# Performance work log

Hardware: AMD Instinct MI355X
Metric: run time of the kernel (lower is better)

## Reference

```python
import jax, jax.numpy as jnp
import numpy as np

N_NODES = 50000
N_EDGES = 800000

def _gcn_layer(x, W, b, src, dst, n):
    # DGL GraphConv, norm='both': out = D_in^{-1/2} A D_out^{-1/2} x W + b
    e = src.shape[0]
    ones = jnp.ones((e,), dtype=x.dtype)
    deg_out = jax.ops.segment_sum(ones, src, num_segments=n)
    deg_in = jax.ops.segment_sum(ones, dst, num_segments=n)
    norm_src = jax.lax.rsqrt(jnp.clip(deg_out, 1.0))  # [n]
    norm_dst = jax.lax.rsqrt(jnp.clip(deg_in, 1.0))   # [n]
    # weight applied before aggregation (in_feats >= out_feats path in DGL)
    h = (x * norm_src[:, None]) @ W                   # [n, out]
    agg = jax.ops.segment_sum(h[src], dst, num_segments=n)  # SpMM: gather-scatter
    return agg * norm_dst[:, None] + b

def setup_inputs() -> dict:
    key = jax.random.key(0)
    ks = jax.random.split(key, 7)
    d_in, d_hid, d_out = 512, 256, 128
    features = jax.random.normal(ks[0], (N_NODES, d_in), dtype=jnp.float32)
    src = jax.random.randint(ks[1], (N_EDGES,), 0, N_NODES, dtype=jnp.int64)
    dst = jax.random.randint(ks[2], (N_EDGES,), 0, N_NODES, dtype=jnp.int64)
    W1 = jax.random.normal(ks[3], (d_in, d_hid), dtype=jnp.float32) / np.sqrt(d_in)
    b1 = jnp.zeros((d_hid,), dtype=jnp.float32)
    W2 = jax.random.normal(ks[4], (d_hid, d_out), dtype=jnp.float32) / np.sqrt(d_hid)
    b2 = jnp.zeros((d_out,), dtype=jnp.float32)
    return {"features": features, "src": src, "dst": dst,
            "W1": W1, "b1": b1, "W2": W2, "b2": b2}

def reference(features, src, dst, W1, b1, W2, b2):
    n = features.shape[0]
    x = _gcn_layer(features, W1, b1, src, dst, n)
    x = jax.nn.relu(x)
    x = _gcn_layer(x, W2, b2, src, dst, n)
    return x
```

## Files before the change

kernel.cpp:

```cpp
#include <hip/hip_runtime.h>
#include <type_traits>

#define DIN  512
#define DHID 256
#define DOF  128

#define RB   13
#define RSZ  (1 << RB)
#define BPR  32

typedef _Float16 f16;
typedef _Float16 f16x8 __attribute__((ext_vector_type(8)));
typedef float f32x4 __attribute__((ext_vector_type(4)));

__global__ __launch_bounds__(256) void hist_deg(const int* __restrict__ src,
                                                const int* __restrict__ dst, int e,
                                                int* __restrict__ cnt_out,
                                                int* __restrict__ cnt_in) {
    __shared__ int h_out[RSZ], h_in[RSZ];
    const int r = blockIdx.x / BPR, b = blockIdx.x % BPR;
    const int base = r << RB;
    const int tid = threadIdx.x;
    for (int j = tid; j < RSZ; j += 256) { h_out[j] = 0; h_in[j] = 0; }
    __syncthreads();

    const int ce = (((e + BPR - 1) / BPR) + 3) & ~3;
    const int s0 = b * ce, s1 = min(s0 + ce, e);
    for (int i = s0 + tid * 4; i < s1; i += 1024) {
        if (i + 3 < s1) {
            int4 sv = *(const int4*)(src + i);
            int4 dv = *(const int4*)(dst + i);
            int v;
            v = sv.x - base; if ((unsigned)v < RSZ) atomicAdd(&h_out[v], 1);
            v = sv.y - base; if ((unsigned)v < RSZ) atomicAdd(&h_out[v], 1);
            v = sv.z - base; if ((unsigned)v < RSZ) atomicAdd(&h_out[v], 1);
            v = sv.w - base; if ((unsigned)v < RSZ) atomicAdd(&h_out[v], 1);
            v = dv.x - base; if ((unsigned)v < RSZ) atomicAdd(&h_in[v], 1);
            v = dv.y - base; if ((unsigned)v < RSZ) atomicAdd(&h_in[v], 1);
            v = dv.z - base; if ((unsigned)v < RSZ) atomicAdd(&h_in[v], 1);
            v = dv.w - base; if ((unsigned)v < RSZ) atomicAdd(&h_in[v], 1);
        } else {
            for (int q = i; q < s1; ++q) {
                int v = src[q] - base; if ((unsigned)v < RSZ) atomicAdd(&h_out[v], 1);
                v = dst[q] - base;     if ((unsigned)v < RSZ) atomicAdd(&h_in[v], 1);
            }
        }
    }
    __syncthreads();
    int* co = cnt_out + (size_t)(r * BPR + b) * RSZ;
    int* ci = cnt_in  + (size_t)(r * BPR + b) * RSZ;
    for (int j = tid; j < RSZ; j += 256) { co[j] = h_out[j]; ci[j] = h_in[j]; }
}

__global__ void sum_base(const int* __restrict__ cnt_out, int* __restrict__ cnt_in,
                         int* __restrict__ deg_in,
                         float* __restrict__ norm_src, float* __restrict__ norm_dst, int n) {
    int d = blockIdx.x * blockDim.x + threadIdx.x;
    if (d >= n) return;
    const int r = d >> RB, j = d & (RSZ - 1);
    int* ci = cnt_in + (size_t)(r * BPR) * RSZ + j;
    int s = 0;
#pragma unroll 4
    for (int b = 0; b < BPR; ++b) {
        int c = ci[(size_t)b * RSZ];
        ci[(size_t)b * RSZ] = s;
        s += c;
    }
    deg_in[d] = s;
    norm_dst[d] = rsqrtf(fmaxf((float)s, 1.0f));
    const int* co = cnt_out + (size_t)(r * BPR) * RSZ + j;
    int s2 = 0;
#pragma unroll 4
    for (int b = 0; b < BPR; ++b) s2 += co[(size_t)b * RSZ];
    norm_src[d] = rsqrtf(fmaxf((float)s2, 1.0f));
}

__global__ __launch_bounds__(256) void scan_part(const int* __restrict__ deg,
                                                 int* __restrict__ partial, int n) {
    const int base = blockIdx.x * 1024;
    const int tid = threadIdx.x;
    int v = 0;
#pragma unroll
    for (int j = 0; j < 4; ++j) {
        int i = base + tid * 4 + j;
        if (i < n) v += deg[i];
    }
    for (int o = 1; o < 64; o <<= 1) v += __shfl_xor(v, o);
    __shared__ int wsum[4];
    if ((tid & 63) == 0) wsum[tid >> 6] = v;
    __syncthreads();
    if (tid == 0) partial[blockIdx.x] = wsum[0] + wsum[1] + wsum[2] + wsum[3];
}

__global__ __launch_bounds__(64) void scan_offsets(int* __restrict__ partial, int nb,
                                                   int* __restrict__ rowptr, int n) {
    const int l = threadIdx.x;
    int orig = (l < nb) ? partial[l] : 0;
    int v = orig;
    for (int o = 1; o < 64; o <<= 1) {
        int u = __shfl_up(v, o);
        if (l >= o) v += u;
    }
    if (l < nb) partial[l] = v - orig;
    if (l == nb - 1) rowptr[n] = v;
}

__global__ __launch_bounds__(256) void scan_apply(const int* __restrict__ deg,
                                                  const int* __restrict__ partial,
                                                  int* __restrict__ rowptr, int n) {
    const int base = blockIdx.x * 1024;
    const int tid = threadIdx.x;
    int x[4]; int s = 0;
#pragma unroll
    for (int j = 0; j < 4; ++j) {
        int i = base + tid * 4 + j;
        x[j] = (i < n) ? deg[i] : 0;
        s += x[j];
    }
    const int l = tid & 63, w = tid >> 6;
    int inc = s;
    for (int o = 1; o < 64; o <<= 1) {
        int u = __shfl_up(inc, o);
        if (l >= o) inc += u;
    }
    __shared__ int wsum[4];
    if (l == 63) wsum[w] = inc;
    __syncthreads();
    int wbase = 0;
    for (int q = 0; q < w; ++q) wbase += wsum[q];
    int excl = partial[blockIdx.x] + wbase + (inc - s);
#pragma unroll
    for (int j = 0; j < 4; ++j) {
        int i = base + tid * 4 + j;
        if (i < n) rowptr[i] = excl;
        excl += x[j];
    }
}

__global__ __launch_bounds__(256) void fill_csr2(const int* __restrict__ src,
                                                 const int* __restrict__ dst, int e,
                                                 const int* __restrict__ rowptr,
                                                 const int* __restrict__ base_in,
                                                 int* __restrict__ csr_src) {
    __shared__ int cur[RSZ];
    const int r = blockIdx.x / BPR, b = blockIdx.x % BPR;
    const int base = r << RB;
    const int tid = threadIdx.x;
    for (int j = tid; j < RSZ; j += 256) cur[j] = 0;
    __syncthreads();

    const int* bi = base_in + (size_t)(r * BPR + b) * RSZ;
    const int ce = (((e + BPR - 1) / BPR) + 3) & ~3;
    const int s0 = b * ce, s1 = min(s0 + ce, e);
    for (int i = s0 + tid * 4; i < s1; i += 1024) {
        if (i + 3 < s1) {
            int4 dv = *(const int4*)(dst + i);
            int4 sv = *(const int4*)(src + i);
            int v;
            v = dv.x - base; if ((unsigned)v < RSZ) { int p = atomicAdd(&cur[v], 1); csr_src[rowptr[base + v] + bi[v] + p] = sv.x; }
            v = dv.y - base; if ((unsigned)v < RSZ) { int p = atomicAdd(&cur[v], 1); csr_src[rowptr[base + v] + bi[v] + p] = sv.y; }
            v = dv.z - base; if ((unsigned)v < RSZ) { int p = atomicAdd(&cur[v], 1); csr_src[rowptr[base + v] + bi[v] + p] = sv.z; }
            v = dv.w - base; if ((unsigned)v < RSZ) { int p = atomicAdd(&cur[v], 1); csr_src[rowptr[base + v] + bi[v] + p] = sv.w; }
        } else {
            for (int q = i; q < s1; ++q) {
                int v = dst[q] - base;
                if ((unsigned)v < RSZ) { int p = atomicAdd(&cur[v], 1); csr_src[rowptr[base + v] + bi[v] + p] = src[q]; }
            }
        }
    }
}

__global__ void transpose_w(const float* __restrict__ W1, const float* __restrict__ W2,
                            f16* __restrict__ w1t, f16* __restrict__ w2t) {
    int t = blockIdx.x * blockDim.x + threadIdx.x;
    if (t < DIN * DHID) {
        int k = t / DHID, c = t % DHID;
        w1t[c * DIN + k] = (f16)W1[t];
    } else {
        int u = t - DIN * DHID;
        if (u < DHID * DOF) {
            int k = u / DOF, c = u % DOF;
            w2t[c * DHID + k] = (f16)W2[u];
        }
    }
}

template<int K, int N, bool A_F32>
__global__ __launch_bounds__(256) void mfma_gemm(const void* __restrict__ Aptr,
                                                 const float* __restrict__ norm,
                                                 const f16* __restrict__ Bt,
                                                 f16* __restrict__ H, int M) {
    constexpr int BM = 128, BN = 128, BK = 32;
    constexpr int NT = K / BK;
    __shared__ __align__(16) f16 smem[BM * BN];

    const int rbase = blockIdx.x * BM;
    const int nbj = blockIdx.y * BN;
    const int tid = threadIdx.x;
    const int l = tid & 63, wid = tid >> 6;
    const int wr = wid >> 1, wc = wid & 1;
    const int fr = l & 15, kg = l >> 4;

    int arow[2], achk[2];
    float ascale[2];
#pragma unroll
    for (int j = 0; j < 2; ++j) {
        int u = tid + j * 256;
        arow[j] = u >> 2; achk[j] = u & 3;
        if (A_F32) {
            int grow = rbase + arow[j];
            ascale[j] = (grow < M) ? norm[grow] : 0.0f;
        }
    }

    struct ABregs {
        float4 a0[2], a1[2];
        f16x8  a16[2];
        f16x8  b[2];
    };

    auto gload = [&](int k0) {
        ABregs r;
#pragma unroll
        for (int j = 0; j < 2; ++j) {
            int grow = rbase + arow[j];
            if (A_F32) {
                if (grow < M) {
                    const float* A = (const float*)Aptr + (long)grow * K + k0 + achk[j] * 8;
                    r.a0[j] = *(const float4*)A;
                    r.a1[j] = *(const float4*)(A + 4);
                } else {
                    r.a0[j] = make_float4(0.f, 0.f, 0.f, 0.f);
                    r.a1[j] = make_float4(0.f, 0.f, 0.f, 0.f);
                }
            } else {
                f16x8 v = {};
                if (grow < M)
                    v = *(const f16x8*)((const f16*)Aptr + (long)grow * K + k0 + achk[j] * 8);
                r.a16[j] = v;
            }
            r.b[j] = *(const f16x8*)(Bt + (long)(nbj + arow[j]) * K + k0 + achk[j] * 8);
        }
        return r;
    };

    auto swrite = [&](int buf, const ABregs& r) {
        f16* As = smem + buf * 8192;
        f16* Bs = As + 4096;
#pragma unroll
        for (int j = 0; j < 2; ++j) {
            f16x8 v;
            if (A_F32) {
                float s = ascale[j];
                v[0] = (f16)(r.a0[j].x * s); v[1] = (f16)(r.a0[j].y * s);
                v[2] = (f16)(r.a0[j].z * s); v[3] = (f16)(r.a0[j].w * s);
                v[4] = (f16)(r.a1[j].x * s); v[5] = (f16)(r.a1[j].y * s);
                v[6] = (f16)(r.a1[j].z * s); v[7] = (f16)(r.a1[j].w * s);
            } else {
                v = r.a16[j];
            }
            int ia = (arow[j] * BK + achk[j] * 8) ^ ((arow[j] & 7) << 3);
            *(f16x8*)&As[ia] = v;
            *(f16x8*)&Bs[ia] = r.b[j];
        }
    };

    f32x4 acc[4][4] = {};

    auto compute = [&](int buf) {
        const f16* As = smem + buf * 8192;
        const f16* Bs = As + 4096;
        f16x8 af[4], bf[4];
#pragma unroll
        for (int m = 0; m < 4; ++m) {
            int row = wr * 64 + m * 16 + fr;
            int ia = (row * BK + kg * 8) ^ ((row & 7) << 3);
            af[m] = *(const f16x8*)&As[ia];
        }
#pragma unroll
        for (int nf = 0; nf < 4; ++nf) {
            int c = wc * 64 + nf * 16 + fr;
            int ib = (c * BK + kg * 8) ^ ((c & 7) << 3);
            bf[nf] = *(const f16x8*)&Bs[ib];
        }
#pragma unroll
        for (int m = 0; m < 4; ++m)
#pragma unroll
            for (int nf = 0; nf < 4; ++nf)
                acc[m][nf] = __builtin_amdgcn_mfma_f32_16x16x32_f16(af[m], bf[nf], acc[m][nf], 0, 0, 0);
    };

    ABregs rb, rc;
    {
        ABregs ra = gload(0);
        swrite(0, ra);
        rb = gload(BK);
        if (NT > 2) rc = gload(2 * BK);
    }

#pragma unroll
    for (int kt = 0; kt < NT; kt += 2) {
        __syncthreads();
        compute(0);
        if (kt + 1 < NT) swrite(1, rb);
        if (kt + 3 < NT) rb = gload((kt + 3) * BK);
        if (kt + 1 < NT) {
            __syncthreads();
            compute(1);
            if (kt + 2 < NT) swrite(0, rc);
            if (kt + 4 < NT) rc = gload((kt + 4) * BK);
        }
    }

    __syncthreads();
#pragma unroll
    for (int m = 0; m < 4; ++m)
#pragma unroll
        for (int nf = 0; nf < 4; ++nf)
#pragma unroll
            for (int i = 0; i < 4; ++i) {
                int row = wr * 64 + m * 16 + (l >> 4) * 4 + i;
                int col = wc * 64 + nf * 16 + (l & 15);
                smem[row * BN + col] = (f16)acc[m][nf][i];
            }
    __syncthreads();
#pragma unroll
    for (int j = 0; j < 8; ++j) {
        int u = tid + j * 256;
        int row = u >> 4, cu = u & 15;
        int grow = rbase + row;
        if (grow < M)
            *(f16x8*)(H + (long)grow * N + nbj + cu * 8) =
                *(const f16x8*)&smem[row * BN + cu * 8];
    }
}

template<int F, bool RELU, bool FOLD, bool OUT_F16>
__global__ __launch_bounds__(256) void aggregate_vec(const f16* __restrict__ H,
                                                     const int* __restrict__ rowptr,
                                                     const int* __restrict__ csr_src,
                                                     const float* __restrict__ norm_dst,
                                                     const float* __restrict__ norm_src,
                                                     const float* __restrict__ bias,
                                                     void* __restrict__ outp, int n) {
    constexpr int LR = F / 8;
    constexpr int EPW = 64 / LR;

    const int node = blockIdx.x * 4 + (threadIdx.x >> 6);
    if (node >= n) return;
    const int l = threadIdx.x & 63;
    const int slot = l / LR;
    const int col = (l & (LR - 1)) * 8;
    const f16* __restrict__ Hc = H + col;

    int k = rowptr[node];
    const int end = rowptr[node + 1];

    float acc[8] = {};
    for (; k + 4 * EPW <= end; k += 4 * EPW) {
        int i0 = csr_src[k + slot];
        int i1 = csr_src[k + EPW + slot];
        int i2 = csr_src[k + 2 * EPW + slot];
        int i3 = csr_src[k + 3 * EPW + slot];
        f16x8 v0 = *(const f16x8*)(Hc + (long)i0 * F);
        f16x8 v1 = *(const f16x8*)(Hc + (long)i1 * F);
        f16x8 v2 = *(const f16x8*)(Hc + (long)i2 * F);
        f16x8 v3 = *(const f16x8*)(Hc + (long)i3 * F);
#pragma unroll
        for (int q = 0; q < 8; ++q) acc[q] += (float)v0[q];
#pragma unroll
        for (int q = 0; q < 8; ++q) acc[q] += (float)v1[q];
#pragma unroll
        for (int q = 0; q < 8; ++q) acc[q] += (float)v2[q];
#pragma unroll
        for (int q = 0; q < 8; ++q) acc[q] += (float)v3[q];
    }
    for (; k < end; k += EPW) {
        int idx = k + slot;
        int ci = min(idx, end - 1);
        int s = csr_src[ci];
        f16x8 v = *(const f16x8*)(Hc + (long)s * F);
        if (idx < end) {
#pragma unroll
            for (int q = 0; q < 8; ++q) acc[q] += (float)v[q];
        }
    }

#pragma unroll
    for (int o = LR; o < 64; o <<= 1) {
#pragma unroll
        for (int q = 0; q < 8; ++q) acc[q] += __shfl_xor(acc[q], o);
    }

    const float nd = norm_dst[node];
    const float ns = FOLD ? norm_src[node] : 1.0f;
#pragma unroll
    for (int q = 0; q < 8; ++q) {
        float v = acc[q] * nd + bias[col + q];
        if (RELU) v = fmaxf(v, 0.0f);
        acc[q] = v * ns;
    }

    if (slot == 0) {
        if (OUT_F16) {
            f16x8 o;
#pragma unroll
            for (int q = 0; q < 8; ++q) o[q] = (f16)acc[q];
            *(f16x8*)((f16*)outp + (long)node * F + col) = o;
        } else {
            float* op = (float*)outp + (long)node * F + col;
            *(float4*)op = make_float4(acc[0], acc[1], acc[2], acc[3]);
            *(float4*)(op + 4) = make_float4(acc[4], acc[5], acc[6], acc[7]);
        }
    }
}

extern "C" void kernel_launch(void* const* d_in, const int* in_sizes, int n_in,
                              void* d_out, int out_size, void* d_ws, size_t ws_size,
                              hipStream_t stream) {
    const float* features = (const float*)d_in[0];
    const int*   src      = (const int*)d_in[1];
    const int*   dst      = (const int*)d_in[2];
    const float* W1       = (const float*)d_in[3];
    const float* b1       = (const float*)d_in[4];
    const float* W2       = (const float*)d_in[5];
    const float* b2       = (const float*)d_in[6];
    float* out = (float*)d_out;

    const int n = in_sizes[0] / DIN;
    const int e = in_sizes[1];

    const int ranges = (n + RSZ - 1) >> RB;
    const size_t cntsz = (size_t)ranges * BPR * RSZ;

    char* ws = (char*)d_ws;
    size_t off = 0;
    auto alloc = [&](size_t bytes) { size_t o = off; off += (bytes + 255) & ~(size_t)255; return o; };
    size_t o_degi   = alloc((size_t)n * 4);
    size_t o_nsrc   = alloc((size_t)n * 4);
    size_t o_ndst   = alloc((size_t)n * 4);
    size_t o_rowptr = alloc((size_t)(n + 1) * 4);
    size_t o_part   = alloc((size_t)64 * 4);
    size_t o_csr    = alloc((size_t)e * 4);
    size_t o_cnto   = alloc(cntsz * 4);
    size_t o_cnti   = alloc(cntsz * 4);
    size_t o_w1t    = alloc((size_t)DIN * DHID * 2);
    size_t o_w2t    = alloc((size_t)DHID * DOF * 2);
    size_t o_h1     = alloc((size_t)n * DHID * 2);
    size_t o_x1     = alloc((size_t)n * DHID * 2);
    size_t o_h2     = alloc((size_t)n * DOF * 2);
    (void)ws_size;

    int*   deg_in   = (int*)(ws + o_degi);
    float* norm_src = (float*)(ws + o_nsrc);
    float* norm_dst = (float*)(ws + o_ndst);
    int*   rowptr   = (int*)(ws + o_rowptr);
    int*   partial  = (int*)(ws + o_part);
    int*   csr_src  = (int*)(ws + o_csr);
    int*   cnt_out  = (int*)(ws + o_cnto);
    int*   cnt_in   = (int*)(ws + o_cnti);
    f16*   w1t      = (f16*)(ws + o_w1t);
    f16*   w2t      = (f16*)(ws + o_w2t);
    f16*   h1       = (f16*)(ws + o_h1);
    f16*   x1       = (f16*)(ws + o_x1);
    f16*   h2       = (f16*)(ws + o_h2);

    const int hblocks = ranges * BPR;
    hist_deg<<<hblocks, 256, 0, stream>>>(src, dst, e, cnt_out, cnt_in);
    sum_base<<<(n + 255) / 256, 256, 0, stream>>>(cnt_out, cnt_in, deg_in,
                                                  norm_src, norm_dst, n);
    const int nb = (n + 1023) / 1024;
    scan_part<<<nb, 256, 0, stream>>>(deg_in, partial, n);
    scan_offsets<<<1, 64, 0, stream>>>(partial, nb, rowptr, n);
    scan_apply<<<nb, 256, 0, stream>>>(deg_in, partial, rowptr, n);
    fill_csr2<<<hblocks, 256, 0, stream>>>(src, dst, e, rowptr, cnt_in, csr_src);
    transpose_w<<<(DIN * DHID + DHID * DOF + 255) / 256, 256, 0, stream>>>(W1, W2, w1t, w2t);

    const int mtiles = (n + 127) / 128;
    const int ablocks = (n + 3) / 4;

    mfma_gemm<DIN, DHID, true><<<dim3(mtiles, DHID / 128), 256, 0, stream>>>(
        features, norm_src, w1t, h1, n);
    aggregate_vec<DHID, true, true, true><<<ablocks, 256, 0, stream>>>(
        h1, rowptr, csr_src, norm_dst, norm_src, b1, x1, n);

    mfma_gemm<DHID, DOF, false><<<dim3(mtiles, DOF / 128), 256, 0, stream>>>(
        x1, nullptr, w2t, h2, n);
    aggregate_vec<DOF, false, false, false><<<ablocks, 256, 0, stream>>>(
        h2, rowptr, csr_src, norm_dst, norm_src, b2, out, n);
}
```

Before: 210.9 us.

## Add LDS-direct double-buffered f16 GEMM for layer 2 and deepen gather unroll

Adds a specialised f16-input GEMM for the second layer that stages A and B tiles straight into LDS with global_load_lds and double buffers them, so loads overlap with MFMA compute. The x1 buffer is padded to a multiple of 128 rows so the kernel can read full tiles without bounds checks. The aggregation loop is also unrolled to 8 outstanding gathers per iteration to expose more memory-level parallelism. The padded rows of x1 are never written, so the GEMM reads uninitialised memory for them; only the output rows beyond n are affected, and those are masked on store. The wider unroll also raises register pressure.

```diff
diff --git a/kernel.cpp b/kernel.cpp
--- a/kernel.cpp
+++ b/kernel.cpp
@@ -12,6 +12,12 @@
 typedef _Float16 f16;
 typedef _Float16 f16x8 __attribute__((ext_vector_type(8)));
 typedef float f32x4 __attribute__((ext_vector_type(4)));
+
+__device__ inline void gload16(const void* g, void* l) {
+    __builtin_amdgcn_global_load_lds(
+        (const __attribute__((address_space(1))) void*)g,
+        (__attribute__((address_space(3))) void*)l, 16, 0, 0);
+}
 
 __global__ __launch_bounds__(256) void hist_deg(const int* __restrict__ src,
                                                 const int* __restrict__ dst, int e,
@@ -335,6 +341,87 @@
     }
 }
 
+template<int K, int N>
+__global__ __launch_bounds__(256) void mfma_gemm16(const f16* __restrict__ A,
+                                                   const f16* __restrict__ Bt,
+                                                   f16* __restrict__ H, int M) {
+    constexpr int BK = 32, NT = K / BK;
+    __shared__ __align__(16) f16 smem[16384];
+    const int rbase = blockIdx.x * 128;
+    const int nbj = blockIdx.y * 128;
+    const int tid = threadIdx.x;
+    const int l = tid & 63, wid = tid >> 6;
+    const int wr = wid >> 1, wc = wid & 1;
+    const int fr = l & 15, kg = l >> 4;
+
+    const int slot0 = wid * 2;
+    const int srow = l >> 2, skch = l & 3;
+
+    auto stage = [&](int buf, int k0) {
+        f16* As = smem + buf * 8192;
+        f16* Bs = As + 4096;
+#pragma unroll
+        for (int q = 0; q < 2; ++q) {
+            int slot = slot0 + q;
+            int row = slot * 16 + srow;
+            const f16* ga = A + (long)(rbase + row) * K + k0 + skch * 8;
+            gload16(ga, As + slot * 512);
+            const f16* gb = Bt + (long)(nbj + row) * K + k0 + skch * 8;
+            gload16(gb, Bs + slot * 512);
+        }
+    };
+
+    f32x4 acc[4][4] = {};
+
+    auto compute = [&](int buf) {
+        const f16* As = smem + buf * 8192;
+        const f16* Bs = As + 4096;
+        f16x8 af[4], bf[4];
+#pragma unroll
+        for (int m = 0; m < 4; ++m)
+            af[m] = *(const f16x8*)&As[(wr * 64 + m * 16 + fr) * 32 + kg * 8];
+#pragma unroll
+        for (int nf = 0; nf < 4; ++nf)
+            bf[nf] = *(const f16x8*)&Bs[(wc * 64 + nf * 16 + fr) * 32 + kg * 8];
+#pragma unroll
+        for (int m = 0; m < 4; ++m)
+#pragma unroll
+            for (int nf = 0; nf < 4; ++nf)
+                acc[m][nf] = __builtin_amdgcn_mfma_f32_16x16x32_f16(af[m], bf[nf], acc[m][nf], 0, 0, 0);
+    };
+
+    stage(0, 0);
+    __syncthreads();
+    int buf = 0;
+    for (int kt = 0; kt < NT; ++kt) {
+        if (kt + 1 < NT) stage(buf ^ 1, (kt + 1) * BK);
+        compute(buf);
+        __syncthreads();
+        buf ^= 1;
+    }
+
+#pragma unroll
+    for (int m = 0; m < 4; ++m)
+#pragma unroll
+        for (int nf = 0; nf < 4; ++nf)
+#pragma unroll
+            for (int i = 0; i < 4; ++i) {
+                int row = wr * 64 + m * 16 + (l >> 4) * 4 + i;
+                int col = wc * 64 + nf * 16 + (l & 15);
+                smem[row * 128 + col] = (f16)acc[m][nf][i];
+            }
+    __syncthreads();
+#pragma unroll
+    for (int j = 0; j < 8; ++j) {
+        int u = tid + j * 256;
+        int row = u >> 4, cu = u & 15;
+        int grow = rbase + row;
+        if (grow < M)
+            *(f16x8*)(H + (long)grow * N + nbj + cu * 8) =
+                *(const f16x8*)&smem[row * 128 + cu * 8];
+    }
+}
+
 template<int F, bool RELU, bool FOLD, bool OUT_F16>
 __global__ __launch_bounds__(256) void aggregate_vec(const f16* __restrict__ H,
                                                      const int* __restrict__ rowptr,
@@ -357,23 +444,27 @@
     const int end = rowptr[node + 1];
 
     float acc[8] = {};
-    for (; k + 4 * EPW <= end; k += 4 * EPW) {
+    for (; k + 8 * EPW <= end; k += 8 * EPW) {
+        int id[8];
+#pragma unroll
+        for (int b = 0; b < 8; ++b) id[b] = csr_src[k + b * EPW + slot];
+        f16x8 v[8];
+#pragma unroll
+        for (int b = 0; b < 8; ++b) v[b] = *(const f16x8*)(Hc + (long)id[b] * F);
+#pragma unroll
+        for (int b = 0; b < 8; ++b)
+#pragma unroll
+            for (int q = 0; q < 8; ++q) acc[q] += (float)v[b][q];
+    }
+    for (; k + 2 * EPW <= end; k += 2 * EPW) {
         int i0 = csr_src[k + slot];
         int i1 = csr_src[k + EPW + slot];
-        int i2 = csr_src[k + 2 * EPW + slot];
-        int i3 = csr_src[k + 3 * EPW + slot];
         f16x8 v0 = *(const f16x8*)(Hc + (long)i0 * F);
         f16x8 v1 = *(const f16x8*)(Hc + (long)i1 * F);
-        f16x8 v2 = *(const f16x8*)(Hc + (long)i2 * F);
-        f16x8 v3 = *(const f16x8*)(Hc + (long)i3 * F);
 #pragma unroll
         for (int q = 0; q < 8; ++q) acc[q] += (float)v0[q];
 #pragma unroll
         for (int q = 0; q < 8; ++q) acc[q] += (float)v1[q];
-#pragma unroll
-        for (int q = 0; q < 8; ++q) acc[q] += (float)v2[q];
-#pragma unroll
-        for (int q = 0; q < 8; ++q) acc[q] += (float)v3[q];
     }
     for (; k < end; k += EPW) {
         int idx = k + slot;
@@ -429,6 +520,7 @@
 
     const int n = in_sizes[0] / DIN;
     const int e = in_sizes[1];
+    const int mpad = (n + 127) & ~127;
 
     const int ranges = (n + RSZ - 1) >> RB;
     const size_t cntsz = (size_t)ranges * BPR * RSZ;
@@ -447,7 +539,7 @@
     size_t o_w1t    = alloc((size_t)DIN * DHID * 2);
     size_t o_w2t    = alloc((size_t)DHID * DOF * 2);
     size_t o_h1     = alloc((size_t)n * DHID * 2);
-    size_t o_x1     = alloc((size_t)n * DHID * 2);
+    size_t o_x1     = alloc((size_t)mpad * DHID * 2);
     size_t o_h2     = alloc((size_t)n * DOF * 2);
     (void)ws_size;
 
@@ -484,8 +576,7 @@
     aggregate_vec<DHID, true, true, true><<<ablocks, 256, 0, stream>>>(
         h1, rowptr, csr_src, norm_dst, norm_src, b1, x1, n);
 
-    mfma_gemm<DHID, DOF, false><<<dim3(mtiles, DOF / 128), 256, 0, stream>>>(
-        x1, nullptr, w2t, h2, n);
+    mfma_gemm16<DHID, DOF><<<dim3(mpad / 128, DOF / 128), 256, 0, stream>>>(x1, w2t, h2, n);
     aggregate_vec<DOF, false, false, false><<<ablocks, 256, 0, stream>>>(
         h2, rowptr, csr_src, norm_dst, norm_src, b2, out, n);
 }
```

New measurement: 216.4 us. +2.6%, slower.
